# Kernel tuning notes

Hardware: AMD Instinct MI355X
Metric: run time of the kernel (lower is better)

## Reference

```python
import jax, jax.numpy as jnp
import numpy as np

# --- basis bookkeeping (mirrors TwoBodyToSpherical._generate_buffers) ---
METADATA = np.array([3, 2, 1], dtype=np.int64)          # shells per l
N_IRREPS = 2 * np.arange(3, dtype=np.int64) + 1          # 2l+1
REP_OFFSETS = np.concatenate([[0], np.cumsum(METADATA * N_IRREPS)[:-1]])
NUM_REPS_1D = int((METADATA * N_IRREPS).sum())           # = 14
M_IDX_MAP = {0: [0], 1: [0, 2, 1], 2: [0, 1, 2, 3, 4]}
ANGULAR = {"s": 0, "p": 1, "d": 2}

C_AOS = ["1s", "2s", "3s"] + ["2p"] * 3 + ["3p"] * 3 + ["3d"] * 5
H_AOS = ["1s", "2s"]


def _build_repid_map(aos):
    # faithful port of the per-element repid_map construction (valence_only=True)
    repid = np.zeros(len(aos), dtype=np.int64)
    dst_n, l_last, m_qc = 0, 0, 0
    for i, ao in enumerate(aos):
        l = ANGULAR[ao[1]]
        if l > l_last:
            dst_n = 0
        repid[i] = REP_OFFSETS[l] + dst_n + M_IDX_MAP[l][m_qc] * METADATA[l]
        if m_qc == 2 * l:
            m_qc = 0
            dst_n += 1
        else:
            m_qc += 1
        l_last = l
    return repid


def setup_inputs() -> dict:
    key = jax.random.key(0)
    maps = {"C": _build_repid_map(C_AOS), "H": _build_repid_map(H_AOS)}
    atomsybs = ["C"] * 400 + ["H"] * 100               # 500 atoms
    n_atoms = len(atomsybs)
    dst_rep_ids_1d = np.concatenate([maps[a] for a in atomsybs])
    lens = np.array([len(maps[a]) for a in atomsybs], dtype=np.int64)
    dst_offsets_1d = np.repeat(np.arange(n_atoms, dtype=np.int64), lens)
    dst_flat_ids_1d = dst_offsets_1d * NUM_REPS_1D + dst_rep_ids_1d  # [N_ao]=5800
    n_ao = dst_flat_ids_1d.shape[0]
    feat_ten = jax.random.normal(key, (n_ao, n_ao), dtype=jnp.float32)
    return {
        "feat_ten": feat_ten,
        "dst_flat_ids_1d": jnp.asarray(dst_flat_ids_1d, dtype=jnp.int32),
        "n_atoms": n_atoms,
        "num_reps_1d": NUM_REPS_1D,
    }


def reference(feat_ten, dst_flat_ids_1d, n_atoms, num_reps_1d):
    total = n_atoms * num_reps_1d                        # 7000
    # 2D destination flat ids: outer-sum of 1D ids (rep_dims=(0,1))
    ids2d = (dst_flat_ids_1d[:, None] * total + dst_flat_ids_1d[None, :]).reshape(-1)
    flat = feat_ten.reshape(-1)
    out_flat = jnp.zeros((total * total,), dtype=feat_ten.dtype).at[ids2d].add(flat)
    # view(n_atoms, R, n_atoms, R) then transpose(1,2) -> [A, A, R, R]
    out = out_flat.reshape(n_atoms, num_reps_1d, n_atoms, num_reps_1d)
    return jnp.transpose(out, (0, 2, 1, 3))
```

## Files before the change

### kernel.cpp

```cpp
#include <hip/hip_runtime.h>

constexpr int R = 14;
constexpr int A = 500;
constexpr int TOTAL = A * R;
constexpr int TILE = R * R;
constexpr int G = 25;
constexpr int NG = A / G;
constexpr int SUPER = 4;
constexpr int NSUP = NG / SUPER;
constexpr int WP = 364;
constexpr int CHUNK = G * TILE;
constexpr int SENT = (int)0xC0000000;

typedef float v4f __attribute__((ext_vector_type(4)));

__global__ __launch_bounds__(1024) void setup_kernel(
        const int* __restrict__ dst, int n_ao,
        int* __restrict__ inv, int* __restrict__ arow,
        int* __restrict__ ncols, int* __restrict__ pm) {
    int tid = threadIdx.x;
    for (int t = tid; t < TOTAL; t += 1024) inv[t] = -1;
    __syncthreads();
    for (int t = tid; t < n_ao; t += 1024) inv[dst[t]] = t;
    __syncthreads();
    if (tid < A) {
        int a = tid, lo = 0x7fffffff, hi = -1;
#pragma unroll
        for (int r = 0; r < R; ++r) {
            int v = inv[a * R + r];
            if (v >= 0) { lo = min(lo, v); hi = max(hi, v); }
        }
        arow[a] = lo;
        ncols[a] = hi - lo + 1;
#pragma unroll
        for (int r = 0; r < R; ++r) {
            int v = inv[a * R + r];
            pm[a * R + r] = (v >= 0) ? (v - lo) : -1;
        }
    }
}

__global__ __launch_bounds__(512, 8) void tile_kernel(
        const float* __restrict__ feat,
        const int* __restrict__ arow,
        const int* __restrict__ ncols,
        const int* __restrict__ pm,
        float* __restrict__ out, int n_ao) {
    const int gs  = blockIdx.x % NSUP;
    const int a1  = blockIdx.x / NSUP;
    const int tid = threadIdx.x;

    __shared__ float buf[R * WP];
    __shared__ int s_pc[SUPER][G * R];
    __shared__ int s_off[SUPER][G];

    const int arow1 = arow[a1];
    const int n1    = ncols[a1];
    const int gbase = gs * (SUPER * G);

    for (int t = tid; t < SUPER * G * R; t += 512) {
        const int pmv = pm[gbase * R + t];
        (&s_pc[0][0])[t] = (pmv >= 0) ? pmv : SENT;
    }
    if (tid < SUPER * G) {
        const int sI = tid / G, i = tid - sI * G;
        const int g0 = gbase + sI * G;
        s_off[sI][i] = arow[g0 + i] - (arow[g0] & ~3);
    }

    int rb_[3][4], ci_[3][4], a2i_[3];
    bool val_[3];
#pragma unroll
    for (int j = 0; j < 3; ++j) {
        const int o4 = tid * 4 + j * 2048;
        val_[j] = (o4 < CHUNK);
        const int o = val_[j] ? o4 : 0;
        int a2i = o / TILE;
        int e   = o - a2i * TILE;
        int r1  = e / R;
        int r2  = e - r1 * R;
        a2i_[j] = a2i;
#pragma unroll
        for (int k = 0; k < 4; ++k) {
            const int dd = pm[a1 * R + r1];
            rb_[j][k] = (dd >= 0) ? dd * WP : SENT;
            ci_[j][k] = a2i * R + r2;
            if (++r2 == R) { r2 = 0; ++r1; }
        }
    }

    const int d0  = tid >> 7;
    const int c4  = tid & 127;
    const int rs4 = n_ao >> 2;

    auto stage = [&](int s) {
        const int g0   = gbase + s * G;
        const int colA = arow[g0] & ~3;
        const int W4   = (arow[g0 + G - 1] + ncols[g0 + G - 1] - colA + 3) >> 2;
        if (c4 < W4) {
            const v4f* src = reinterpret_cast<const v4f*>(feat)
                           + (long long)arow1 * rs4 + (colA >> 2) + c4;
#pragma unroll
            for (int u = 0; u < 4; ++u) {
                const int d = d0 + u * 4;
                if (d < n1)
                    *reinterpret_cast<v4f*>(&buf[d * WP + (c4 << 2)]) =
                        __builtin_nontemporal_load(src + (long long)d * rs4);
            }
        }
    };

    auto emit = [&](int s) {
        const long long outbase =
            ((long long)a1 * A + gbase + s * G) * (long long)TILE;
        const int* pcS = &s_pc[s][0];
#pragma unroll
        for (int j = 0; j < 3; ++j) {
            if (!val_[j]) continue;
            const int off = s_off[s][a2i_[j]];
            v4f v;
#pragma unroll
            for (int k = 0; k < 4; ++k) {
                const int c   = pcS[ci_[j][k]];
                const int idx = rb_[j][k] + off + c;
                const float x = buf[max(idx, 0)];
                ((float*)&v)[k] = (idx >= 0) ? x : 0.0f;
            }
            __builtin_nontemporal_store(
                v, reinterpret_cast<v4f*>(out + outbase + tid * 4 + j * 2048));
        }
    };

    stage(0);
    __syncthreads();
    for (int s = 0; s < SUPER; ++s) {
        emit(s);
        if (s + 1 < SUPER) {
            __syncthreads();
            stage(s + 1);
            __syncthreads();
        }
    }
}

extern "C" void kernel_launch(void* const* d_in, const int* in_sizes, int n_in,
                              void* d_out, int out_size, void* d_ws, size_t ws_size,
                              hipStream_t stream) {
    const float* feat = (const float*)d_in[0];
    const int*   dst  = (const int*)d_in[1];
    int n_ao = in_sizes[1];

    int* inv   = (int*)d_ws;
    int* arow  = inv + TOTAL;
    int* ncols = arow + A;
    int* pm    = ncols + A;

    setup_kernel<<<1, 1024, 0, stream>>>(dst, n_ao, inv, arow, ncols, pm);
    tile_kernel<<<A * NSUP, 512, 0, stream>>>(feat, arow, ncols, pm,
                                              (float*)d_out, n_ao);
}
```

Baseline: 302.2 us.

## Prefetch next stage into registers during emit and fold offsets into LDS table

Global loads for the next column group are now issued into registers before the current group is emitted, then written to LDS after the barrier, so load latency overlaps the gather-and-store work. The per-group column offset is also folded into a single combined shared-memory table, removing one LDS read and an add per element. The cost is more registers per thread for the prefetch buffers, which could lower occupancy under the 512x8 launch bounds.

Measured after the change: 300.2 us. About the same (-0.6%).

```diff
diff --git a/kernel.cpp b/kernel.cpp
--- a/kernel.cpp
+++ b/kernel.cpp
@@ -51,24 +51,21 @@
     const int tid = threadIdx.x;
 
     __shared__ float buf[R * WP];
-    __shared__ int s_pc[SUPER][G * R];
-    __shared__ int s_off[SUPER][G];
+    __shared__ int s_cof[SUPER * G * R];
 
     const int arow1 = arow[a1];
     const int n1    = ncols[a1];
     const int gbase = gs * (SUPER * G);
 
     for (int t = tid; t < SUPER * G * R; t += 512) {
-        const int pmv = pm[gbase * R + t];
-        (&s_pc[0][0])[t] = (pmv >= 0) ? pmv : SENT;
-    }
-    if (tid < SUPER * G) {
-        const int sI = tid / G, i = tid - sI * G;
-        const int g0 = gbase + sI * G;
-        s_off[sI][i] = arow[g0 + i] - (arow[g0] & ~3);
+        const int i    = t / R;
+        const int a2   = gbase + i;
+        const int colA = arow[gbase + (i / G) * G] & ~3;
+        const int pmv  = pm[gbase * R + t];
+        s_cof[t] = (pmv >= 0) ? (arow[a2] - colA + pmv) : SENT;
     }
 
-    int rb_[3][4], ci_[3][4], a2i_[3];
+    int rb_[3][4], ci_[3][4];
     bool val_[3];
 #pragma unroll
     for (int j = 0; j < 3; ++j) {
@@ -79,7 +76,6 @@
         int e   = o - a2i * TILE;
         int r1  = e / R;
         int r2  = e - r1 * R;
-        a2i_[j] = a2i;
 #pragma unroll
         for (int k = 0; k < 4; ++k) {
             const int dd = pm[a1 * R + r1];
@@ -93,7 +89,9 @@
     const int c4  = tid & 127;
     const int rs4 = n_ao >> 2;
 
-    auto stage = [&](int s) {
+    v4f rg[4];
+
+    auto issue_loads = [&](int s) {
         const int g0   = gbase + s * G;
         const int colA = arow[g0] & ~3;
         const int W4   = (arow[g0 + G - 1] + ncols[g0 + G - 1] - colA + 3) >> 2;
@@ -104,8 +102,20 @@
             for (int u = 0; u < 4; ++u) {
                 const int d = d0 + u * 4;
                 if (d < n1)
-                    *reinterpret_cast<v4f*>(&buf[d * WP + (c4 << 2)]) =
-                        __builtin_nontemporal_load(src + (long long)d * rs4);
+                    rg[u] = __builtin_nontemporal_load(src + (long long)d * rs4);
+            }
+        }
+    };
+    auto write_lds = [&](int s) {
+        const int g0   = gbase + s * G;
+        const int colA = arow[g0] & ~3;
+        const int W4   = (arow[g0 + G - 1] + ncols[g0 + G - 1] - colA + 3) >> 2;
+        if (c4 < W4) {
+#pragma unroll
+            for (int u = 0; u < 4; ++u) {
+                const int d = d0 + u * 4;
+                if (d < n1)
+                    *reinterpret_cast<v4f*>(&buf[d * WP + (c4 << 2)]) = rg[u];
             }
         }
     };
@@ -113,16 +123,15 @@
     auto emit = [&](int s) {
         const long long outbase =
             ((long long)a1 * A + gbase + s * G) * (long long)TILE;
-        const int* pcS = &s_pc[s][0];
+        const int* pcS = &s_cof[s * G * R];
 #pragma unroll
         for (int j = 0; j < 3; ++j) {
             if (!val_[j]) continue;
-            const int off = s_off[s][a2i_[j]];
             v4f v;
 #pragma unroll
             for (int k = 0; k < 4; ++k) {
-                const int c   = pcS[ci_[j][k]];
-                const int idx = rb_[j][k] + off + c;
+                const int cof = pcS[ci_[j][k]];
+                const int idx = rb_[j][k] + cof;
                 const float x = buf[max(idx, 0)];
                 ((float*)&v)[k] = (idx >= 0) ? x : 0.0f;
             }
@@ -131,13 +140,15 @@
         }
     };
 
-    stage(0);
+    issue_loads(0);
+    write_lds(0);
     __syncthreads();
     for (int s = 0; s < SUPER; ++s) {
+        if (s + 1 < SUPER) issue_loads(s + 1);
         emit(s);
         if (s + 1 < SUPER) {
             __syncthreads();
-            stage(s + 1);
+            write_lds(s + 1);
             __syncthreads();
         }
     }
```
